# Kernel optimization log

Hardware: AMD Instinct MI355X
Metric: run time of the kernel (lower is better)

The kernel has to match this reference:

```python
import jax, jax.numpy as jnp
import numpy as np

LEAKY_ALPHA = 0.2
LN_EPS = 1e-5


def setup_inputs() -> dict:
    key = jax.random.key(0)
    ks = jax.random.split(key, 6)
    B, N, D, R, Hh, hd = 2, 2048, 128, 3, 4, 32  # head_dim = out_dim // num_heads = 128 // 4
    H = jax.random.normal(ks[0], (B, N, D), dtype=jnp.float32)
    A = jax.random.randint(ks[1], (R, B, N, N), 0, 2, dtype=jnp.int32)  # 0/1 adjacency per relation
    w_scale = float(np.sqrt(2.0 / (D + hd)))  # xavier-like
    a_scale = float(np.sqrt(2.0 / (hd + 1)))
    W = jax.random.normal(ks[2], (R, Hh, D, hd), dtype=jnp.float32) * w_scale
    a_src = jax.random.normal(ks[3], (R, Hh, hd), dtype=jnp.float32) * a_scale
    a_dst = jax.random.normal(ks[4], (R, Hh, hd), dtype=jnp.float32) * a_scale
    ln_gamma = jnp.ones((D,), dtype=jnp.float32)
    ln_beta = jnp.zeros((D,), dtype=jnp.float32)
    return {"H": H, "A": A, "W": W, "a_src": a_src, "a_dst": a_dst,
            "ln_gamma": ln_gamma, "ln_beta": ln_beta}


def reference(H, A, W, a_src, a_dst, ln_gamma, ln_beta):
    # H: [B,N,D]; A: [R,B,N,N] int; W: [R,Hh,D,hd]; a_*: [R,Hh,hd]
    R = W.shape[0]
    B, N, D = H.shape
    mask = (A > 0)[:, :, None, :, :]                    # [R,B,1,N,N]
    Wh = jnp.einsum('bnd,rhdf->rbhnf', H, W)             # [R,B,Hh,N,hd]
    e_src = jnp.einsum('rbhnf,rhf->rbhn', Wh, a_src)
    e_dst = jnp.einsum('rbhnf,rhf->rbhn', Wh, a_dst)
    e = e_src[..., :, None] + e_dst[..., None, :]        # [R,B,Hh,N,N]
    e = jax.nn.leaky_relu(e, LEAKY_ALPHA)
    all_false = ~jnp.any(mask, axis=-1, keepdims=True)   # rows with empty neighborhood
    logits = jnp.where(mask, e, -jnp.inf)
    logits = jnp.where(all_false, 0.0, logits)           # avoid NaN on empty rows
    alpha = jax.nn.softmax(logits, axis=-1)
    alpha = jnp.where(all_false, 0.0, alpha)
    # attention-weighted aggregation, mean over relations; -> [B,N,Hh,hd]
    agg = jnp.einsum('rbhij,rbhjf->bihf', alpha, Wh) / R
    out = agg.reshape(B, N, -1)                          # concat heads -> [B,N,out_dim]
    x = H + out                                          # res_proj is Identity (in_dim==out_dim); dropout in eval
    mu = jnp.mean(x, axis=-1, keepdims=True)
    var = jnp.var(x, axis=-1, keepdims=True)
    return (x - mu) / jnp.sqrt(var + LN_EPS) * ln_gamma + ln_beta
```

## Files before the change

### kernel.cpp

```cpp
#include <hip/hip_runtime.h>
#include <hip/hip_bf16.h>

#define RR 3
#define BB 2
#define NN 2048
#define DD 128
#define HH 4
#define HD 32
#define LEAKY 0.2f
#define LN_EPS 1e-5f
#define LOG2E 1.4426950408889634f

using f32x4  = __attribute__((ext_vector_type(4))) float;
using bf16x8 = __attribute__((ext_vector_type(8))) short;

__device__ __forceinline__ void gload_lds16(const void* g, void* l) {
    __builtin_amdgcn_global_load_lds(
        (const __attribute__((address_space(1))) unsigned*)g,
        (__attribute__((address_space(3))) unsigned*)l, 16, 0, 0);
}
__device__ __forceinline__ void gload_lds4(const void* g, void* l) {
    __builtin_amdgcn_global_load_lds(
        (const __attribute__((address_space(1))) unsigned*)g,
        (__attribute__((address_space(3))) unsigned*)l, 4, 0, 0);
}

__global__ __launch_bounds__(256) void compact_kernel(
    const int* __restrict__ A, unsigned* __restrict__ bm,
    const float* __restrict__ H, __hip_bfloat16* __restrict__ Hb)
{
    const int bid = blockIdx.x;
    if (bid < 16) {
        const int row = bid * 256 + threadIdx.x;
        const float4* src = (const float4*)(H + (long)row * DD);
        ushort4* dst = (ushort4*)(Hb + (long)row * DD);
#pragma unroll
        for (int k = 0; k < 32; ++k) {
            float4 v = src[k];
            ushort4 o;
            o.x = __builtin_bit_cast(unsigned short, __float2bfloat16(v.x));
            o.y = __builtin_bit_cast(unsigned short, __float2bfloat16(v.y));
            o.z = __builtin_bit_cast(unsigned short, __float2bfloat16(v.z));
            o.w = __builtin_bit_cast(unsigned short, __float2bfloat16(v.w));
            dst[k] = o;
        }
        return;
    }
    const int cb = bid - 16;
    const int wave = cb * 4 + ((int)threadIdx.x >> 6);
    const int lane = threadIdx.x & 63;
    const long base = (long)wave * 2048;
    const int* Ap = A + base;
    unsigned word = 0;
#pragma unroll
    for (int e = 0; e < 32; ++e) {
        const int v = Ap[e * 64 + lane];
        const unsigned long long bal = __ballot(v != 0);
        if ((lane >> 1) == e)
            word = (lane & 1) ? (unsigned)(bal >> 32) : (unsigned)bal;
    }
    bm[(base >> 5) + lane] = word;
}

__global__ __launch_bounds__(256) void wh_kernel(
    const __hip_bfloat16* __restrict__ Hb, const float* __restrict__ W,
    const float* __restrict__ a_src, const float* __restrict__ a_dst,
    float* __restrict__ es, float* __restrict__ ed,
    __hip_bfloat16* __restrict__ whT)
{
    const int bid = blockIdx.x;
    const int rbh = bid >> 4;
    const int nch = bid & 15;
    const int h = rbh & 3;
    const int b = (rbh >> 2) & 1;
    const int r = rbh >> 3;
    const int wi = r * HH + h;
    const int w  = threadIdx.x >> 6;
    const int l  = threadIdx.x & 63;
    const int lr = l & 15;
    const int lg = l >> 4;

    const float* Wp = W + (long)wi * DD * HD;
    bf16x8 afr[2][4];
#pragma unroll
    for (int mt = 0; mt < 2; ++mt)
#pragma unroll
        for (int kt = 0; kt < 4; ++kt)
#pragma unroll
            for (int e = 0; e < 8; ++e) {
                const float wv = Wp[(kt * 32 + lg * 8 + e) * HD + mt * 16 + lr];
                afr[mt][kt][e] = __builtin_bit_cast(short, __float2bfloat16(wv));
            }

    float av[2][4], dv[2][4];
#pragma unroll
    for (int mt = 0; mt < 2; ++mt)
#pragma unroll
        for (int reg = 0; reg < 4; ++reg) {
            const int f = mt * 16 + lg * 4 + reg;
            av[mt][reg] = a_src[wi * HD + f] * LOG2E;
            dv[mt][reg] = a_dst[wi * HD + f] * LOG2E;
        }

#pragma unroll
    for (int nt = 0; nt < 2; ++nt) {
        const int ncol = nch * 128 + w * 32 + nt * 16 + lr;
        const __hip_bfloat16* hrow = Hb + ((long)b * NN + ncol) * DD;
        f32x4 acc0 = {0.f, 0.f, 0.f, 0.f};
        f32x4 acc1 = {0.f, 0.f, 0.f, 0.f};
#pragma unroll
        for (int kt = 0; kt < 4; ++kt) {
            bf16x8 bfr = *(const bf16x8*)(hrow + kt * 32 + lg * 8);
            acc0 = __builtin_amdgcn_mfma_f32_16x16x32_bf16(afr[0][kt], bfr, acc0, 0, 0, 0);
            acc1 = __builtin_amdgcn_mfma_f32_16x16x32_bf16(afr[1][kt], bfr, acc1, 0, 0, 0);
        }
        float s = 0.f, d = 0.f;
#pragma unroll
        for (int reg = 0; reg < 4; ++reg) {
            const int f0 = lg * 4 + reg;
            const int f1 = 16 + lg * 4 + reg;
            whT[((long)rbh * HD + f0) * NN + ncol] = __float2bfloat16(acc0[reg]);
            whT[((long)rbh * HD + f1) * NN + ncol] = __float2bfloat16(acc1[reg]);
            s = fmaf(acc0[reg], av[0][reg], s);
            s = fmaf(acc1[reg], av[1][reg], s);
            d = fmaf(acc0[reg], dv[0][reg], d);
            d = fmaf(acc1[reg], dv[1][reg], d);
        }
        s += __shfl_xor(s, 16); s += __shfl_xor(s, 32);
        d += __shfl_xor(d, 16); d += __shfl_xor(d, 32);
        if (l < 16) {
            es[(long)rbh * NN + ncol] = s;
            ed[(long)rbh * NN + ncol] = d;
        }
    }
}

__global__ __launch_bounds__(256, 3) void gat_attn_kernel(
    const unsigned* __restrict__ bm, const float* __restrict__ es,
    const float* __restrict__ ed, const __hip_bfloat16* __restrict__ whT,
    float* __restrict__ num, float* __restrict__ den)
{
    const int lg = ((int)blockIdx.x % 8) * 96 + (int)blockIdx.x / 8;
    const int jh = lg & 1;
    const int it = (lg >> 1) & 15;
    const int h  = (lg >> 5) & 3;
    const int b  = (lg >> 7) & 1;
    const int r  = lg >> 8;
    const int i0 = it << 7;
    const int tid = threadIdx.x;
    const int w = tid >> 6;
    const int l = tid & 63;
    const int row = l & 15;
    const int kg  = l >> 4;
    const int f31 = l & 31;
    const int kgr = l >> 5;

    __shared__ __align__(16) short    whs[2][4][4][32][8];
    __shared__ __align__(16) unsigned bms[2][4][128];
    __shared__ __align__(16) float    eds[2][4][32];
    __shared__ float red[4];

    const int rbh = (r * BB + b) * HH + h;
    const long rbNN = (long)(r * BB + b) * NN;
    const __hip_bfloat16* whTr = whT + (long)rbh * HD * NN;
    const float* edr = ed + (long)rbh * NN;
    const int jbase = jh * (NN / 2);

#define STAGE(s, nb) do {                                                           \
        const int j0s = jbase + (s) * 128;                                          \
        gload_lds16(whTr + (long)f31 * NN + j0s + w * 32 + kgr * 8,                 \
                    &whs[nb][w][0][0][0]);                                          \
        gload_lds16(whTr + (long)f31 * NN + j0s + w * 32 + (2 + kgr) * 8,           \
                    &whs[nb][w][2][0][0]);                                          \
        gload_lds4(bm + (rbNN + i0 + l) * (NN / 32) + (j0s >> 5) + w,               \
                   &bms[nb][w][0]);                                                 \
        gload_lds4(bm + (rbNN + i0 + 64 + l) * (NN / 32) + (j0s >> 5) + w,          \
                   &bms[nb][w][64]);                                                \
        if (l < 32) gload_lds4(edr + j0s + w * 32 + l, &eds[nb][w][0]);             \
    } while (0)

    STAGE(0, 0);

    float4 m0 = ((const float4*)edr)[tid * 2];
    float4 m1 = ((const float4*)edr)[tid * 2 + 1];
    float mm = fmaxf(fmaxf(fmaxf(m0.x, m0.y), fmaxf(m0.z, m0.w)),
                     fmaxf(fmaxf(m1.x, m1.y), fmaxf(m1.z, m1.w)));
#pragma unroll
    for (int d = 1; d < 64; d <<= 1) mm = fmaxf(mm, __shfl_xor(mm, d));
    if (l == 0) red[w] = mm;
    __syncthreads();
    const float medf = fmaxf(fmaxf(red[0], red[1]), fmaxf(red[2], red[3]));

    const float esvA = es[(long)rbh * NN + i0 + w * 16 + row];
    const float esvB = es[(long)rbh * NN + i0 + 64 + w * 16 + row];
    const float xA = esvA + medf, xB = esvB + medf;
    const float MA = fmaxf(xA, LEAKY * xA), MB = fmaxf(xB, LEAKY * xB);
    const float uA = esvA - MA, vA = fmaf(LEAKY, esvA, -MA);
    const float uB = esvB - MB, vB = fmaf(LEAKY, esvB, -MB);

    f32x4 acc0A = {0,0,0,0}, acc1A = {0,0,0,0}, accDA = {0,0,0,0};
    f32x4 acc0B = {0,0,0,0}, acc1B = {0,0,0,0}, accDB = {0,0,0,0};
    bf16x8 ones;
#pragma unroll
    for (int i = 0; i < 8; ++i) ones[i] = (short)0x3F80;

    for (int s = 0; s < 8; ++s) {
        const int cb = s & 1, nb = cb ^ 1;
        if (s < 7) {
            STAGE(s + 1, nb);
            asm volatile("s_waitcnt vmcnt(5)" ::: "memory");
        } else {
            asm volatile("s_waitcnt vmcnt(0)" ::: "memory");
        }
        __builtin_amdgcn_s_barrier();
        __builtin_amdgcn_sched_barrier(0);

#pragma unroll
        for (int jc = 0; jc < 4; ++jc) {
            bf16x8 b0 = *(const bf16x8*)&whs[cb][jc][kg][row][0];
            bf16x8 b1 = *(const bf16x8*)&whs[cb][jc][kg][row + 16][0];
            float4 e0 = *(const float4*)&eds[cb][jc][kg * 8];
            float4 e1 = *(const float4*)&eds[cb][jc][kg * 8 + 4];
            const unsigned mybA = (bms[cb][jc][w * 16 + row] >> (kg * 8)) & 0xffu;
            const unsigned mybB = (bms[cb][jc][64 + w * 16 + row] >> (kg * 8)) & 0xffu;

            float ev[8];
            ev[0] = e0.x; ev[1] = e0.y; ev[2] = e0.z; ev[3] = e0.w;
            ev[4] = e1.x; ev[5] = e1.y; ev[6] = e1.z; ev[7] = e1.w;

            bf16x8 pA, pB;
#pragma unroll
            for (int c = 0; c < 8; ++c) {
                float pa = __builtin_amdgcn_exp2f(
                    fmaxf(uA + ev[c], fmaf(LEAKY, ev[c], vA)));
                float pb = __builtin_amdgcn_exp2f(
                    fmaxf(uB + ev[c], fmaf(LEAKY, ev[c], vB)));
                const int ma = ((int)(mybA << (31 - c))) >> 31;
                const int mb = ((int)(mybB << (31 - c))) >> 31;
                pa = __uint_as_float(__float_as_uint(pa) & (unsigned)ma);
                pb = __uint_as_float(__float_as_uint(pb) & (unsigned)mb);
                __hip_bfloat16 ha = __float2bfloat16(pa);
                __hip_bfloat16 hb = __float2bfloat16(pb);
                pA[c] = __builtin_bit_cast(short, ha);
                pB[c] = __builtin_bit_cast(short, hb);
            }

            acc0A = __builtin_amdgcn_mfma_f32_16x16x32_bf16(pA, b0, acc0A, 0, 0, 0);
            acc1A = __builtin_amdgcn_mfma_f32_16x16x32_bf16(pA, b1, acc1A, 0, 0, 0);
            accDA = __builtin_amdgcn_mfma_f32_16x16x32_bf16(pA, ones, accDA, 0, 0, 0);
            acc0B = __builtin_amdgcn_mfma_f32_16x16x32_bf16(pB, b0, acc0B, 0, 0, 0);
            acc1B = __builtin_amdgcn_mfma_f32_16x16x32_bf16(pB, b1, acc1B, 0, 0, 0);
            accDB = __builtin_amdgcn_mfma_f32_16x16x32_bf16(pB, ones, accDB, 0, 0, 0);
        }
        __builtin_amdgcn_s_barrier();
        __builtin_amdgcn_sched_barrier(0);
    }
#undef STAGE

    const int fcol = l & 15;
    const int pr = r * 2 + jh;
#pragma unroll
    for (int reg = 0; reg < 4; ++reg) {
        const int orow = (l >> 4) * 4 + reg;
        const long roA = (long)pr * (BB * NN) + (long)b * NN + i0 + w * 16 + orow;
        const long roB = roA + 64;
        num[roA * DD + h * HD + fcol]      = acc0A[reg];
        num[roA * DD + h * HD + 16 + fcol] = acc1A[reg];
        num[roB * DD + h * HD + fcol]      = acc0B[reg];
        num[roB * DD + h * HD + 16 + fcol] = acc1B[reg];
        if (fcol == 0) {
            den[roA * HH + h] = accDA[reg];
            den[roB * HH + h] = accDB[reg];
        }
    }
}

__global__ __launch_bounds__(256) void finalize_kernel(
    const float* __restrict__ H, const float* __restrict__ num,
    const float* __restrict__ den,
    const float* __restrict__ gamma, const float* __restrict__ beta,
    float* __restrict__ out)
{
    const int w = threadIdx.x >> 6;
    const int l = threadIdx.x & 63;
    const long row = (long)blockIdx.x * 4 + w;
    const float2 hv = ((const float2*)(H + row * DD))[l];

    float ax = 0.f, ay = 0.f;
#pragma unroll
    for (int r = 0; r < RR; ++r) {
        float dsum = 0.f, nx = 0.f, ny = 0.f;
#pragma unroll
        for (int j = 0; j < 2; ++j) {
            const long ro = (long)(r * 2 + j) * (BB * NN) + row;
            dsum += den[ro * HH + (l >> 4)];
            const float2 nv = ((const float2*)(num + ro * DD))[l];
            nx += nv.x; ny += nv.y;
        }
        const float inv = (dsum > 0.f) ? 1.0f / dsum : 0.0f;
        ax = fmaf(nx, inv, ax);
        ay = fmaf(ny, inv, ay);
    }
    const float x0 = hv.x + ax * (1.0f / RR);
    const float x1 = hv.y + ay * (1.0f / RR);
    float s = x0 + x1, q = x0 * x0 + x1 * x1;
#pragma unroll
    for (int m = 1; m < 64; m <<= 1) {
        s += __shfl_xor(s, m);
        q += __shfl_xor(q, m);
    }
    const float mu  = s * (1.0f / DD);
    const float var = q * (1.0f / DD) - mu * mu;
    const float inv = rsqrtf(var + LN_EPS);
    const float g0 = gamma[l * 2], g1 = gamma[l * 2 + 1];
    const float b0 = beta[l * 2],  b1 = beta[l * 2 + 1];
    float2 o;
    o.x = (x0 - mu) * inv * g0 + b0;
    o.y = (x1 - mu) * inv * g1 + b1;
    ((float2*)(out + row * DD))[l] = o;
}

extern "C" void kernel_launch(void* const* d_in, const int* in_sizes, int n_in,
                              void* d_out, int out_size, void* d_ws, size_t ws_size,
                              hipStream_t stream)
{
    const float* H      = (const float*)d_in[0];
    const int*   A      = (const int*)d_in[1];
    const float* W      = (const float*)d_in[2];
    const float* a_src  = (const float*)d_in[3];
    const float* a_dst  = (const float*)d_in[4];
    const float* gamma  = (const float*)d_in[5];
    const float* beta   = (const float*)d_in[6];
    float* out = (float*)d_out;

    char* ws = (char*)d_ws;
    float* num = (float*)ws;                     ws += (size_t)RR * 2 * BB * NN * DD * 4;
    float* den = (float*)ws;                     ws += (size_t)RR * 2 * BB * NN * HH * 4;
    float* es  = (float*)ws;                     ws += (size_t)RR * BB * HH * NN * 4;
    float* ed  = (float*)ws;                     ws += (size_t)RR * BB * HH * NN * 4;
    __hip_bfloat16* whT = (__hip_bfloat16*)ws;   ws += (size_t)RR * BB * HH * HD * NN * 2;
    unsigned* bmask = (unsigned*)ws;             ws += (size_t)RR * BB * NN * (NN / 32) * 4;
    __hip_bfloat16* Hb = (__hip_bfloat16*)ws;    ws += (size_t)BB * NN * DD * 2;

    compact_kernel<<<16 + RR * BB * NN * (NN / 32) / 256, 256, 0, stream>>>(A, bmask, H, Hb);
    wh_kernel<<<24 * 16, 256, 0, stream>>>(Hb, W, a_src, a_dst, es, ed, whT);
    gat_attn_kernel<<<RR * BB * HH * 16 * 2, 256, 0, stream>>>(bmask, es, ed, whT, num, den);
    finalize_kernel<<<BB * NN / 4, 256, 0, stream>>>(H, num, den, gamma, beta, out);
}
```

Measured before the change: 73.50 us.

## Fuse Wh projection into mask compaction kernel and store partial numerators as bf16

The bf16 conversion of H and the Wh projection kernel are merged into one prep kernel that also compacts the adjacency mask. The projection now reads fp32 H directly and converts it in registers, which removes one launch and the Hb intermediate buffer. The attention kernel now writes its partial numerators as packed bf16 pairs instead of fp32, halving that intermediate traffic, and the finalize kernel unpacks them with a remapped column layout. The cost is lower precision in the partial sums and projection blocks that reload H redundantly across relations and heads.

Result: faster. 64.55 us (-12.2%).

```diff
diff --git a/kernel.cpp b/kernel.cpp
--- a/kernel.cpp
+++ b/kernel.cpp
@@ -24,59 +24,46 @@
         (const __attribute__((address_space(1))) unsigned*)g,
         (__attribute__((address_space(3))) unsigned*)l, 4, 0, 0);
 }
-
-__global__ __launch_bounds__(256) void compact_kernel(
-    const int* __restrict__ A, unsigned* __restrict__ bm,
-    const float* __restrict__ H, __hip_bfloat16* __restrict__ Hb)
+__device__ __forceinline__ unsigned short bfb(float x) {
+    return __builtin_bit_cast(unsigned short, __float2bfloat16(x));
+}
+
+__global__ __launch_bounds__(256) void prep_kernel(
+    const float* __restrict__ H, const int* __restrict__ A,
+    const float* __restrict__ W,
+    const float* __restrict__ a_src, const float* __restrict__ a_dst,
+    float* __restrict__ es, float* __restrict__ ed,
+    __hip_bfloat16* __restrict__ whT, unsigned* __restrict__ bm)
 {
     const int bid = blockIdx.x;
-    if (bid < 16) {
-        const int row = bid * 256 + threadIdx.x;
-        const float4* src = (const float4*)(H + (long)row * DD);
-        ushort4* dst = (ushort4*)(Hb + (long)row * DD);
-#pragma unroll
-        for (int k = 0; k < 32; ++k) {
-            float4 v = src[k];
-            ushort4 o;
-            o.x = __builtin_bit_cast(unsigned short, __float2bfloat16(v.x));
-            o.y = __builtin_bit_cast(unsigned short, __float2bfloat16(v.y));
-            o.z = __builtin_bit_cast(unsigned short, __float2bfloat16(v.z));
-            o.w = __builtin_bit_cast(unsigned short, __float2bfloat16(v.w));
-            dst[k] = o;
-        }
+    const int t = threadIdx.x;
+
+    if (bid >= 384) {
+        const int cb = bid - 384;
+        const int wave = cb * 4 + (t >> 6);
+        const int lane = t & 63;
+        const long base = (long)wave * 2048;
+        const int* Ap = A + base;
+        unsigned word = 0;
+#pragma unroll
+        for (int e = 0; e < 32; ++e) {
+            const int v = Ap[e * 64 + lane];
+            const unsigned long long bal = __ballot(v != 0);
+            if ((lane >> 1) == e)
+                word = (lane & 1) ? (unsigned)(bal >> 32) : (unsigned)bal;
+        }
+        bm[(base >> 5) + lane] = word;
         return;
     }
-    const int cb = bid - 16;
-    const int wave = cb * 4 + ((int)threadIdx.x >> 6);
-    const int lane = threadIdx.x & 63;
-    const long base = (long)wave * 2048;
-    const int* Ap = A + base;
-    unsigned word = 0;
-#pragma unroll
-    for (int e = 0; e < 32; ++e) {
-        const int v = Ap[e * 64 + lane];
-        const unsigned long long bal = __ballot(v != 0);
-        if ((lane >> 1) == e)
-            word = (lane & 1) ? (unsigned)(bal >> 32) : (unsigned)bal;
-    }
-    bm[(base >> 5) + lane] = word;
-}
-
-__global__ __launch_bounds__(256) void wh_kernel(
-    const __hip_bfloat16* __restrict__ Hb, const float* __restrict__ W,
-    const float* __restrict__ a_src, const float* __restrict__ a_dst,
-    float* __restrict__ es, float* __restrict__ ed,
-    __hip_bfloat16* __restrict__ whT)
-{
-    const int bid = blockIdx.x;
+
     const int rbh = bid >> 4;
     const int nch = bid & 15;
     const int h = rbh & 3;
     const int b = (rbh >> 2) & 1;
     const int r = rbh >> 3;
     const int wi = r * HH + h;
-    const int w  = threadIdx.x >> 6;
-    const int l  = threadIdx.x & 63;
+    const int w  = t >> 6;
+    const int l  = t & 63;
     const int lr = l & 15;
     const int lg = l >> 4;
 
@@ -87,10 +74,8 @@
 #pragma unroll
         for (int kt = 0; kt < 4; ++kt)
 #pragma unroll
-            for (int e = 0; e < 8; ++e) {
-                const float wv = Wp[(kt * 32 + lg * 8 + e) * HD + mt * 16 + lr];
-                afr[mt][kt][e] = __builtin_bit_cast(short, __float2bfloat16(wv));
-            }
+            for (int e = 0; e < 8; ++e)
+                afr[mt][kt][e] = (short)bfb(Wp[(kt * 32 + lg * 8 + e) * HD + mt * 16 + lr]);
 
     float av[2][4], dv[2][4];
 #pragma unroll
@@ -105,12 +90,18 @@
 #pragma unroll
     for (int nt = 0; nt < 2; ++nt) {
         const int ncol = nch * 128 + w * 32 + nt * 16 + lr;
-        const __hip_bfloat16* hrow = Hb + ((long)b * NN + ncol) * DD;
+        const float4* hrow4 = (const float4*)(H + ((long)b * NN + ncol) * DD);
         f32x4 acc0 = {0.f, 0.f, 0.f, 0.f};
         f32x4 acc1 = {0.f, 0.f, 0.f, 0.f};
 #pragma unroll
         for (int kt = 0; kt < 4; ++kt) {
-            bf16x8 bfr = *(const bf16x8*)(hrow + kt * 32 + lg * 8);
+            float4 h0 = hrow4[kt * 8 + lg * 2];
+            float4 h1 = hrow4[kt * 8 + lg * 2 + 1];
+            bf16x8 bfr;
+            bfr[0] = (short)bfb(h0.x); bfr[1] = (short)bfb(h0.y);
+            bfr[2] = (short)bfb(h0.z); bfr[3] = (short)bfb(h0.w);
+            bfr[4] = (short)bfb(h1.x); bfr[5] = (short)bfb(h1.y);
+            bfr[6] = (short)bfb(h1.z); bfr[7] = (short)bfb(h1.w);
             acc0 = __builtin_amdgcn_mfma_f32_16x16x32_bf16(afr[0][kt], bfr, acc0, 0, 0, 0);
             acc1 = __builtin_amdgcn_mfma_f32_16x16x32_bf16(afr[1][kt], bfr, acc1, 0, 0, 0);
         }
@@ -138,7 +129,7 @@
 __global__ __launch_bounds__(256, 3) void gat_attn_kernel(
     const unsigned* __restrict__ bm, const float* __restrict__ es,
     const float* __restrict__ ed, const __hip_bfloat16* __restrict__ whT,
-    float* __restrict__ num, float* __restrict__ den)
+    unsigned* __restrict__ num, float* __restrict__ den)
 {
     const int lg = ((int)blockIdx.x % 8) * 96 + (int)blockIdx.x / 8;
     const int jh = lg & 1;
@@ -264,10 +255,10 @@
         const int orow = (l >> 4) * 4 + reg;
         const long roA = (long)pr * (BB * NN) + (long)b * NN + i0 + w * 16 + orow;
         const long roB = roA + 64;
-        num[roA * DD + h * HD + fcol]      = acc0A[reg];
-        num[roA * DD + h * HD + 16 + fcol] = acc1A[reg];
-        num[roB * DD + h * HD + fcol]      = acc0B[reg];
-        num[roB * DD + h * HD + 16 + fcol] = acc1B[reg];
+        const unsigned wa = (unsigned)bfb(acc0A[reg]) | ((unsigned)bfb(acc1A[reg]) << 16);
+        const unsigned wb_ = (unsigned)bfb(acc0B[reg]) | ((unsigned)bfb(acc1B[reg]) << 16);
+        num[roA * 64 + h * 16 + fcol] = wa;
+        num[roB * 64 + h * 16 + fcol] = wb_;
         if (fcol == 0) {
             den[roA * HH + h] = accDA[reg];
             den[roB * HH + h] = accDB[reg];
@@ -276,7 +267,7 @@
 }
 
 __global__ __launch_bounds__(256) void finalize_kernel(
-    const float* __restrict__ H, const float* __restrict__ num,
+    const float* __restrict__ H, const unsigned* __restrict__ num,
     const float* __restrict__ den,
     const float* __restrict__ gamma, const float* __restrict__ beta,
     float* __restrict__ out)
@@ -284,7 +275,10 @@
     const int w = threadIdx.x >> 6;
     const int l = threadIdx.x & 63;
     const long row = (long)blockIdx.x * 4 + w;
-    const float2 hv = ((const float2*)(H + row * DD))[l];
+    const int hh = l >> 4, cc = l & 15;
+    const int c_lo = hh * 32 + cc, c_hi = c_lo + 16;
+    const float hx = H[row * DD + c_lo];
+    const float hy = H[row * DD + c_hi];
 
     float ax = 0.f, ay = 0.f;
 #pragma unroll
@@ -293,16 +287,17 @@
 #pragma unroll
         for (int j = 0; j < 2; ++j) {
             const long ro = (long)(r * 2 + j) * (BB * NN) + row;
-            dsum += den[ro * HH + (l >> 4)];
-            const float2 nv = ((const float2*)(num + ro * DD))[l];
-            nx += nv.x; ny += nv.y;
+            dsum += den[ro * HH + hh];
+            const unsigned wv = num[ro * 64 + l];
+            nx += __uint_as_float(wv << 16);
+            ny += __uint_as_float(wv & 0xffff0000u);
         }
         const float inv = (dsum > 0.f) ? 1.0f / dsum : 0.0f;
         ax = fmaf(nx, inv, ax);
         ay = fmaf(ny, inv, ay);
     }
-    const float x0 = hv.x + ax * (1.0f / RR);
-    const float x1 = hv.y + ay * (1.0f / RR);
+    const float x0 = hx + ax * (1.0f / RR);
+    const float x1 = hy + ay * (1.0f / RR);
     float s = x0 + x1, q = x0 * x0 + x1 * x1;
 #pragma unroll
     for (int m = 1; m < 64; m <<= 1) {
@@ -312,12 +307,8 @@
     const float mu  = s * (1.0f / DD);
     const float var = q * (1.0f / DD) - mu * mu;
     const float inv = rsqrtf(var + LN_EPS);
-    const float g0 = gamma[l * 2], g1 = gamma[l * 2 + 1];
-    const float b0 = beta[l * 2],  b1 = beta[l * 2 + 1];
-    float2 o;
-    o.x = (x0 - mu) * inv * g0 + b0;
-    o.y = (x1 - mu) * inv * g1 + b1;
-    ((float2*)(out + row * DD))[l] = o;
+    out[row * DD + c_lo] = (x0 - mu) * inv * gamma[c_lo] + beta[c_lo];
+    out[row * DD + c_hi] = (x1 - mu) * inv * gamma[c_hi] + beta[c_hi];
 }
 
 extern "C" void kernel_launch(void* const* d_in, const int* in_sizes, int n_in,
@@ -334,16 +325,15 @@
     float* out = (float*)d_out;
 
     char* ws = (char*)d_ws;
-    float* num = (float*)ws;                     ws += (size_t)RR * 2 * BB * NN * DD * 4;
+    unsigned* num = (unsigned*)ws;               ws += (size_t)RR * 2 * BB * NN * 64 * 4;
     float* den = (float*)ws;                     ws += (size_t)RR * 2 * BB * NN * HH * 4;
     float* es  = (float*)ws;                     ws += (size_t)RR * BB * HH * NN * 4;
     float* ed  = (float*)ws;                     ws += (size_t)RR * BB * HH * NN * 4;
     __hip_bfloat16* whT = (__hip_bfloat16*)ws;   ws += (size_t)RR * BB * HH * HD * NN * 2;
     unsigned* bmask = (unsigned*)ws;             ws += (size_t)RR * BB * NN * (NN / 32) * 4;
-    __hip_bfloat16* Hb = (__hip_bfloat16*)ws;    ws += (size_t)BB * NN * DD * 2;
-
-    compact_kernel<<<16 + RR * BB * NN * (NN / 32) / 256, 256, 0, stream>>>(A, bmask, H, Hb);
-    wh_kernel<<<24 * 16, 256, 0, stream>>>(Hb, W, a_src, a_dst, es, ed, whT);
+
+    prep_kernel<<<384 + RR * BB * NN * (NN / 32) / 256, 256, 0, stream>>>(
+        H, A, W, a_src, a_dst, es, ed, whT, bmask);
     gat_attn_kernel<<<RR * BB * HH * 16 * 2, 256, 0, stream>>>(bmask, es, ed, whT, num, den);
     finalize_kernel<<<BB * NN / 4, 256, 0, stream>>>(H, num, den, gamma, beta, out);
 }
```
